# Performance work log

Hardware: AMD Instinct MI355X
Metric: run time of the kernel (lower is better)

Reference implementation:

```python
import jax, jax.numpy as jnp
import numpy as np

N_HEADS = 4
D_K = 64

def setup_inputs() -> dict:
    key = jax.random.key(0)
    k1, k2, k3 = jax.random.split(key, 3)
    B, C, H, W = 16, 256, 32, 32
    x = jax.random.normal(k1, (B, C, H, W), dtype=jnp.float32)
    # Linear(C, 3*n_heads*d_k) stored as [in, out] for x @ W
    w_proj = jax.random.normal(k2, (C, 3 * N_HEADS * D_K), dtype=jnp.float32) * (1.0 / np.sqrt(C))
    b_proj = jnp.zeros((3 * N_HEADS * D_K,), dtype=jnp.float32)
    w_out = jax.random.normal(k3, (N_HEADS * D_K, C), dtype=jnp.float32) * (1.0 / np.sqrt(N_HEADS * D_K))
    b_out = jnp.zeros((C,), dtype=jnp.float32)
    return {"x": x, "w_proj": w_proj, "b_proj": b_proj, "w_out": w_out, "b_out": b_out}

def reference(x, w_proj, b_proj, w_out, b_out):
    B, C, H, W = x.shape
    S = H * W
    scale = D_K ** -0.5
    xs = x.reshape(B, C, S).transpose(0, 2, 1)            # [B, S, C]
    qkv = (xs @ w_proj + b_proj).reshape(B, S, N_HEADS, 3 * D_K)
    q, k, v = jnp.split(qkv, 3, axis=3)                    # each [B, S, H, dk]
    attn = jnp.einsum('bihd,bjhd->bijh', q, k) * scale     # [B, S, S, heads]
    attn = jax.nn.softmax(attn, axis=2)
    o = jnp.einsum('bijh,bjhd->bihd', attn, v)             # [B, S, heads, dk]
    o = o.reshape(B, S, N_HEADS * D_K)
    res = o @ w_out + b_out + xs                           # [B, S, C]
    return res.transpose(0, 2, 1).reshape(B, C, H, W)
```

## Files before the change

kernel.cpp:

```cpp
#include <hip/hip_runtime.h>
#include <math.h>

#define B_  16
#define C_  256
#define S_  1024
#define NH  4
#define DK  64
#define P3  768
#define ND  256

typedef unsigned short u16;
typedef unsigned int   u32;
typedef float  f32x4  __attribute__((ext_vector_type(4)));
typedef short  bf16x8 __attribute__((ext_vector_type(8)));

#define MFMA16(a, b, c) __builtin_amdgcn_mfma_f32_16x16x32_bf16(a, b, c, 0, 0, 0)

#define QSCALE 0.1803368801111137f

#define WAITVM(N) asm volatile("s_waitcnt vmcnt(" #N ")" ::: "memory")
#define BARRIER() asm volatile("s_barrier" ::: "memory")

__device__ __forceinline__ u16 f2bf(float f) {
    union { float f; u32 u; } x; x.f = f;
    u32 r = x.u + 0x7fffu + ((x.u >> 16) & 1u);
    return (u16)(r >> 16);
}

__device__ __forceinline__ void stage16(const u16* g, u16* l) {
    __builtin_amdgcn_global_load_lds(
        (const __attribute__((address_space(1))) void*)g,
        (__attribute__((address_space(3))) void*)l, 16, 0, 0);
}

__global__ __launch_bounds__(256) void transpose_all(
    const float* __restrict__ x, u16* __restrict__ xt,
    const float* __restrict__ wp, u16* __restrict__ wpT,
    const float* __restrict__ wo, u16* __restrict__ woT)
{
    const int z = blockIdx.z;
    const float* src;
    u16* dst;
    int Cc;
    if (z < 16)       { src = x + (size_t)z * C_ * S_; dst = xt + (size_t)z * C_ * S_; Cc = S_; }
    else if (z == 16) { src = wp; dst = wpT; Cc = P3; }
    else              { src = wo; dst = woT; Cc = ND; }
    if ((int)blockIdx.x * 64 >= Cc) return;
    const int R = C_;

    __shared__ float T[64][65];
    const int tid = threadIdx.x;
    const int c0 = blockIdx.x * 64, r0 = blockIdx.y * 64;

    const int l64 = tid & 63, rr0 = tid >> 6;
    #pragma unroll
    for (int t = 0; t < 16; ++t) {
        int rr = rr0 + t * 4;
        T[rr][l64] = src[(size_t)(r0 + rr) * Cc + c0 + l64];
    }
    __syncthreads();
    const int rp = tid & 31;
    const int cb = tid >> 5;
    #pragma unroll
    for (int t = 0; t < 8; ++t) {
        int c = cb + t * 8;
        u32 lo = f2bf(T[2 * rp][c]);
        u32 hi = f2bf(T[2 * rp + 1][c]);
        *(u32*)&dst[(size_t)(c0 + c) * R + r0 + 2 * rp] = lo | (hi << 16);
    }
}

__global__ __launch_bounds__(256) void qkv_mfma(
    const u16* __restrict__ xt, const u16* __restrict__ wpT,
    const float* __restrict__ bp, u16* __restrict__ qo,
    u16* __restrict__ ko, u16* __restrict__ vo)
{
    __shared__ __align__(16) u16 SM[24576];

    const int tid = threadIdx.x;
    const int w = tid >> 6, lane = tid & 63;
    const int n_ = lane & 15, quad = lane >> 4;
    const int n0 = blockIdx.x * 64, s0 = blockIdx.y * 128, b = blockIdx.z;

    const u16* ar0 = xt + ((size_t)b * S_ + s0 + (2 * w + 0) * 16 + n_) * C_ + quad * 8;
    const u16* ar1 = xt + ((size_t)b * S_ + s0 + (2 * w + 1) * 16 + n_) * C_ + quad * 8;
    const u16* br  = wpT + (size_t)(n0 + w * 16 + n_) * C_ + quad * 8;

    f32x4 acc[2][4];
    #pragma unroll
    for (int am = 0; am < 2; ++am)
        #pragma unroll
        for (int nf = 0; nf < 4; ++nf)
            #pragma unroll
            for (int r = 0; r < 4; ++r) acc[am][nf][r] = 0.f;

    {
        u16* As_ = SM;
        u16* Bs_ = SM + 8192;
        stage16(ar0,      As_ + (4 * w + 0) * 512);
        stage16(ar0 + 32, As_ + (4 * w + 1) * 512);
        stage16(ar1,      As_ + (4 * w + 2) * 512);
        stage16(ar1 + 32, As_ + (4 * w + 3) * 512);
        stage16(br,       Bs_ + (2 * w + 0) * 512);
        stage16(br + 32,  Bs_ + (2 * w + 1) * 512);
    }

    #pragma unroll
    for (int p = 0; p < 4; ++p) {
        u16* As_ = SM + (p & 1) * 12288;
        u16* Bs_ = As_ + 8192;
        if (p < 3) {
            const int pk = (p + 1) * 64;
            u16* An = SM + ((p + 1) & 1) * 12288;
            u16* Bn = An + 8192;
            stage16(ar0 + pk,      An + (4 * w + 0) * 512);
            stage16(ar0 + pk + 32, An + (4 * w + 1) * 512);
            stage16(ar1 + pk,      An + (4 * w + 2) * 512);
            stage16(ar1 + pk + 32, An + (4 * w + 3) * 512);
            stage16(br  + pk,      Bn + (2 * w + 0) * 512);
            stage16(br  + pk + 32, Bn + (2 * w + 1) * 512);
            WAITVM(6);
        } else {
            WAITVM(0);
        }
        BARRIER();
        #pragma unroll
        for (int kc = 0; kc < 2; ++kc) {
            bf16x8 af0 = *(const bf16x8*)&As_[((2 * w + 0) * 2 + kc) * 512 + lane * 8];
            bf16x8 af1 = *(const bf16x8*)&As_[((2 * w + 1) * 2 + kc) * 512 + lane * 8];
            #pragma unroll
            for (int nf = 0; nf < 4; ++nf) {
                bf16x8 bf = *(const bf16x8*)&Bs_[(nf * 2 + kc) * 512 + lane * 8];
                acc[0][nf] = MFMA16(af0, bf, acc[0][nf]);
                acc[1][nf] = MFMA16(af1, bf, acc[1][nf]);
            }
        }
        if (p < 3) BARRIER();
    }

    const int hd = n0 / 192, rem = n0 % 192, which = rem / 64;
    const int bh = b * NH + hd;
    float bias[4];
    #pragma unroll
    for (int nf = 0; nf < 4; ++nf) bias[nf] = bp[n0 + nf * 16 + n_];
    const float sc = (which == 0) ? QSCALE : 1.f;

    __syncthreads();
    if (which < 2) {
        u16* Cs = SM;
        #pragma unroll
        for (int am = 0; am < 2; ++am) {
            int row0 = w * 32 + am * 16 + quad * 4;
            #pragma unroll
            for (int nf = 0; nf < 4; ++nf)
                #pragma unroll
                for (int r = 0; r < 4; ++r)
                    Cs[(row0 + r) * 72 + nf * 16 + n_] =
                        f2bf((acc[am][nf][r] + bias[nf]) * sc);
        }
        __syncthreads();
        u16* dst = (which == 0) ? qo : ko;
        #pragma unroll
        for (int t = 0; t < 4; ++t) {
            int ii = tid + t * 256;
            int row = ii >> 3, c8 = (ii & 7) * 8;
            *(bf16x8*)&dst[((size_t)bh * S_ + s0 + row) * DK + c8] =
                *(const bf16x8*)&Cs[row * 72 + c8];
        }
    } else {
        u16* Cs = SM;
        #pragma unroll
        for (int am = 0; am < 2; ++am) {
            int colb = w * 32 + am * 16 + quad * 4;
            #pragma unroll
            for (int nf = 0; nf < 4; ++nf)
                #pragma unroll
                for (int r = 0; r < 4; ++r)
                    Cs[(nf * 16 + n_) * 136 + colb + r] =
                        f2bf(acc[am][nf][r] + bias[nf]);
        }
        __syncthreads();
        #pragma unroll
        for (int t = 0; t < 4; ++t) {
            int ii = tid + t * 256;
            int row = ii >> 4, c8 = (ii & 15) * 8;
            *(bf16x8*)&vo[((size_t)bh * DK + row) * S_ + s0 + c8] =
                *(const bf16x8*)&Cs[row * 136 + c8];
        }
    }
}

__global__ __launch_bounds__(256) void attn_mfma(
    const u16* __restrict__ q, const u16* __restrict__ k,
    const u16* __restrict__ vt, u16* __restrict__ obf)
{
    __shared__ __align__(16) u16 SM[16384];

    const int tid = threadIdx.x;
    const int w = tid >> 6, lane = tid & 63;
    const int n_ = lane & 15, quad = lane >> 4;
    const int i0 = blockIdx.x * 128;
    const int hd = blockIdx.y, b = blockIdx.z;
    const int bh = b * NH + hd;

    bf16x8 qf[2][2];
    #pragma unroll
    for (int am = 0; am < 2; ++am) {
        const u16* qrow = q + ((size_t)bh * S_ + i0 + w * 32 + am * 16 + n_) * DK;
        qf[am][0] = *(const bf16x8*)&qrow[quad * 8];
        qf[am][1] = *(const bf16x8*)&qrow[32 + quad * 8];
    }

    const int kappa = 32 * (w & 1) + 8 * (n_ >> 2) + 4 * (w >> 1) + (n_ & 3);
    const u16* kbase = k  + ((size_t)bh * S_ + kappa) * DK + quad * 8;
    const u16* vbase = vt + ((size_t)bh * DK + w * 16 + n_) * S_ + quad * 8;

    float lsum[2] = {0.f, 0.f};
    f32x4 oacc[2][4];
    #pragma unroll
    for (int am = 0; am < 2; ++am)
        #pragma unroll
        for (int nd = 0; nd < 4; ++nd)
            #pragma unroll
            for (int r = 0; r < 4; ++r) oacc[am][nd][r] = 0.f;

    stage16(kbase,      SM + w * 1024);
    stage16(kbase + 32, SM + w * 1024 + 512);
    stage16(vbase,      SM + 4096 + w * 1024);
    stage16(vbase + 32, SM + 4096 + w * 1024 + 512);

    for (int t = 0; t < 16; ++t) {
        u16* Ks = SM + (t & 1) * 8192;
        u16* Vs = Ks + 4096;
        if (t < 15) {
            const size_t jn = (size_t)(t + 1) * 64;
            u16* Kn = SM + ((t + 1) & 1) * 8192;
            u16* Vn = Kn + 4096;
            stage16(kbase + jn * DK,      Kn + w * 1024);
            stage16(kbase + jn * DK + 32, Kn + w * 1024 + 512);
            stage16(vbase + jn,           Vn + w * 1024);
            stage16(vbase + jn + 32,      Vn + w * 1024 + 512);
            WAITVM(4);
        } else {
            WAITVM(0);
        }
        BARRIER();

        f32x4 sb[2][4];
        __builtin_amdgcn_s_setprio(1);
        #pragma unroll
        for (int nb = 0; nb < 4; ++nb) {
            bf16x8 kf0 = *(const bf16x8*)&Ks[nb * 1024 + lane * 8];
            bf16x8 kf1 = *(const bf16x8*)&Ks[nb * 1024 + 512 + lane * 8];
            #pragma unroll
            for (int am = 0; am < 2; ++am) {
                f32x4 a; a[0] = a[1] = a[2] = a[3] = 0.f;
                a = MFMA16(kf0, qf[am][0], a);
                a = MFMA16(kf1, qf[am][1], a);
                sb[am][nb] = a;
            }
        }
        __builtin_amdgcn_s_setprio(0);

        bf16x8 pa[2][2];
        #pragma unroll
        for (int am = 0; am < 2; ++am) {
            u32 tr[4][4];
            #pragma unroll
            for (int nb = 0; nb < 4; ++nb)
                #pragma unroll
                for (int r = 0; r < 4; ++r) {
                    float p = exp2f(sb[am][nb][r]);
                    u32 bits = __float_as_uint(p) & 0xffff0000u;
                    lsum[am] += __uint_as_float(bits);
                    tr[nb][r] = bits;
                }
            union { bf16x8 v; u32 u[4]; } p0, p1;
            p0.u[0] = (tr[0][0] >> 16) | tr[0][1];
            p0.u[1] = (tr[0][2] >> 16) | tr[0][3];
            p0.u[2] = (tr[2][0] >> 16) | tr[2][1];
            p0.u[3] = (tr[2][2] >> 16) | tr[2][3];
            p1.u[0] = (tr[1][0] >> 16) | tr[1][1];
            p1.u[1] = (tr[1][2] >> 16) | tr[1][3];
            p1.u[2] = (tr[3][0] >> 16) | tr[3][1];
            p1.u[3] = (tr[3][2] >> 16) | tr[3][3];
            pa[am][0] = p0.v;
            pa[am][1] = p1.v;
        }

        __builtin_amdgcn_s_setprio(1);
        #pragma unroll
        for (int nd = 0; nd < 4; ++nd) {
            bf16x8 vf0 = *(const bf16x8*)&Vs[nd * 1024 + lane * 8];
            bf16x8 vf1 = *(const bf16x8*)&Vs[nd * 1024 + 512 + lane * 8];
            #pragma unroll
            for (int am = 0; am < 2; ++am) {
                oacc[am][nd] = MFMA16(vf0, pa[am][0], oacc[am][nd]);
                oacc[am][nd] = MFMA16(vf1, pa[am][1], oacc[am][nd]);
            }
        }
        __builtin_amdgcn_s_setprio(0);

        if (t < 15) BARRIER();
    }

    float inv[2];
    #pragma unroll
    for (int am = 0; am < 2; ++am) {
        float s = lsum[am];
        s += __shfl_xor(s, 16);
        s += __shfl_xor(s, 32);
        inv[am] = 1.f / s;
    }

    __syncthreads();
    u16* eb = SM + w * 2304;
    #pragma unroll
    for (int am = 0; am < 2; ++am)
        #pragma unroll
        for (int nd = 0; nd < 4; ++nd) {
            uint2 uv;
            uv.x = (u32)f2bf(oacc[am][nd][0] * inv[am]) |
                   ((u32)f2bf(oacc[am][nd][1] * inv[am]) << 16);
            uv.y = (u32)f2bf(oacc[am][nd][2] * inv[am]) |
                   ((u32)f2bf(oacc[am][nd][3] * inv[am]) << 16);
            *(uint2*)&eb[(am * 16 + n_) * 72 + nd * 16 + quad * 4] = uv;
        }
    __syncthreads();
    #pragma unroll
    for (int t = 0; t < 4; ++t) {
        int ii = lane + t * 64;
        int row = ii >> 3, c8 = (ii & 7) * 8;
        *(bf16x8*)&obf[((size_t)b * S_ + i0 + w * 32 + row) * ND + hd * DK + c8] =
            *(const bf16x8*)&eb[row * 72 + c8];
    }
}

__global__ __launch_bounds__(256) void out_proj_mfma(
    const u16* __restrict__ obf, const u16* __restrict__ woT,
    const float* __restrict__ bo, const float* __restrict__ x,
    float* __restrict__ out)
{
    __shared__ __align__(16) u16 SM[24576];

    const int tid = threadIdx.x;
    const int w = tid >> 6, lane = tid & 63;
    const int n_ = lane & 15, quad = lane >> 4;
    const int c0 = blockIdx.x * 64, s0 = blockIdx.y * 128, b = blockIdx.z;

    const u16* ar  = woT + (size_t)(c0 + w * 16 + n_) * ND + quad * 8;
    const u16* br0 = obf + ((size_t)b * S_ + s0 + (2 * w + 0) * 16 + n_) * ND + quad * 8;
    const u16* br1 = obf + ((size_t)b * S_ + s0 + (2 * w + 1) * 16 + n_) * ND + quad * 8;

    f32x4 acc[2][4];
    #pragma unroll
    for (int nf = 0; nf < 2; ++nf)
        #pragma unroll
        for (int mb = 0; mb < 4; ++mb)
            #pragma unroll
            for (int r = 0; r < 4; ++r) acc[nf][mb][r] = 0.f;

    {
        u16* Bs_ = SM;
        u16* As_ = SM + 8192;
        stage16(br0,      Bs_ + (4 * w + 0) * 512);
        stage16(br0 + 32, Bs_ + (4 * w + 1) * 512);
        stage16(br1,      Bs_ + (4 * w + 2) * 512);
        stage16(br1 + 32, Bs_ + (4 * w + 3) * 512);
        stage16(ar,       As_ + (2 * w + 0) * 512);
        stage16(ar + 32,  As_ + (2 * w + 1) * 512);
    }

    #pragma unroll
    for (int p = 0; p < 4; ++p) {
        u16* Bs_ = SM + (p & 1) * 12288;
        u16* As_ = Bs_ + 8192;
        if (p < 3) {
            const int pk = (p + 1) * 64;
            u16* Bn = SM + ((p + 1) & 1) * 12288;
            u16* An = Bn + 8192;
            stage16(br0 + pk,      Bn + (4 * w + 0) * 512);
            stage16(br0 + pk + 32, Bn + (4 * w + 1) * 512);
            stage16(br1 + pk,      Bn + (4 * w + 2) * 512);
            stage16(br1 + pk + 32, Bn + (4 * w + 3) * 512);
            stage16(ar  + pk,      An + (2 * w + 0) * 512);
            stage16(ar  + pk + 32, An + (2 * w + 1) * 512);
            WAITVM(6);
        } else {
            WAITVM(0);
        }
        BARRIER();
        #pragma unroll
        for (int kc = 0; kc < 2; ++kc) {
            bf16x8 bf0 = *(const bf16x8*)&Bs_[((2 * w + 0) * 2 + kc) * 512 + lane * 8];
            bf16x8 bf1 = *(const bf16x8*)&Bs_[((2 * w + 1) * 2 + kc) * 512 + lane * 8];
            #pragma unroll
            for (int mb = 0; mb < 4; ++mb) {
                bf16x8 af = *(const bf16x8*)&As_[(mb * 2 + kc) * 512 + lane * 8];
                acc[0][mb] = MFMA16(af, bf0, acc[0][mb]);
                acc[1][mb] = MFMA16(af, bf1, acc[1][mb]);
            }
        }
        if (p < 3) BARRIER();
    }

    #pragma unroll
    for (int mb = 0; mb < 4; ++mb)
        #pragma unroll
        for (int r = 0; r < 4; ++r) {
            int c = c0 + mb * 16 + quad * 4 + r;
            float bias = bo[c];
            #pragma unroll
            for (int nf = 0; nf < 2; ++nf) {
                size_t idx = ((size_t)b * C_ + c) * S_ + s0 + w * 32 + nf * 16 + n_;
                out[idx] = acc[nf][mb][r] + bias + x[idx];
            }
        }
}

extern "C" void kernel_launch(void* const* d_in, const int* in_sizes, int n_in,
                              void* d_out, int out_size, void* d_ws, size_t ws_size,
                              hipStream_t stream) {
    const float* x  = (const float*)d_in[0];
    const float* wp = (const float*)d_in[1];
    const float* bp = (const float*)d_in[2];
    const float* wo = (const float*)d_in[3];
    const float* bo = (const float*)d_in[4];
    float* out = (float*)d_out;

    const size_t QKV_E = (size_t)B_ * NH * S_ * DK;
    u16* q   = (u16*)d_ws;
    u16* kk  = q   + QKV_E;
    u16* vtp = kk  + QKV_E;
    u16* obf = vtp + QKV_E;
    u16* xt  = obf + (size_t)B_ * S_ * ND;
    u16* wpT = xt  + (size_t)B_ * S_ * C_;
    u16* woT = wpT + (size_t)P3 * C_;

    transpose_all<<<dim3(16, 4, 18),             256, 0, stream>>>(x, xt, wp, wpT, wo, woT);
    qkv_mfma     <<<dim3(P3 / 64, S_ / 128, B_), 256, 0, stream>>>(xt, wpT, bp, q, kk, vtp);
    attn_mfma    <<<dim3(S_ / 128, NH, B_),      256, 0, stream>>>(q, kk, vtp, obf);
    out_proj_mfma<<<dim3(C_ / 64, S_ / 128, B_), 256, 0, stream>>>(obf, woT, bo, x, out);
}
```

Baseline: 139.8 us.

## Halve attention query tile to 64 rows, remap blocks per XCD, use packed bf16 convert

Each attention block now handles 64 query rows instead of 128, so each wave owns one 16-row tile and 1024 blocks are launched on a 1D grid. The block index is permuted so consecutive blocks sharing the same (batch, head) K/V land on the same XCD, aiming at better L2 reuse and more parallelism. The manual bf16 truncation and rounding are replaced with the v_cvt_pk_bf16_f32 instruction, and the softmax sum now uses unrounded probabilities. The trade-off is that K/V tiles are loaded twice as often per query row and each wave has less MFMA work per LDS load.

```diff
diff --git a/kernel.cpp b/kernel.cpp
--- a/kernel.cpp
+++ b/kernel.cpp
@@ -25,6 +25,12 @@
     union { float f; u32 u; } x; x.f = f;
     u32 r = x.u + 0x7fffu + ((x.u >> 16) & 1u);
     return (u16)(r >> 16);
+}
+
+__device__ __forceinline__ u32 cvtpk(float lo, float hi) {
+    u32 r;
+    asm("v_cvt_pk_bf16_f32 %0, %1, %2" : "=v"(r) : "v"(lo), "v"(hi));
+    return r;
 }
 
 __device__ __forceinline__ void stage16(const u16* g, u16* l) {
@@ -199,30 +205,31 @@
     const int tid = threadIdx.x;
     const int w = tid >> 6, lane = tid & 63;
     const int n_ = lane & 15, quad = lane >> 4;
-    const int i0 = blockIdx.x * 128;
-    const int hd = blockIdx.y, b = blockIdx.z;
-    const int bh = b * NH + hd;
-
-    bf16x8 qf[2][2];
-    #pragma unroll
-    for (int am = 0; am < 2; ++am) {
-        const u16* qrow = q + ((size_t)bh * S_ + i0 + w * 32 + am * 16 + n_) * DK;
-        qf[am][0] = *(const bf16x8*)&qrow[quad * 8];
-        qf[am][1] = *(const bf16x8*)&qrow[32 + quad * 8];
+
+    const int id  = blockIdx.x;
+    const int nid = (id & 7) * 128 + (id >> 3);
+    const int i0  = (nid & 15) * 64;
+    const int hd  = (nid >> 4) & 3;
+    const int b   = nid >> 6;
+    const int bh  = b * NH + hd;
+
+    bf16x8 qf[2];
+    {
+        const u16* qrow = q + ((size_t)bh * S_ + i0 + w * 16 + n_) * DK;
+        qf[0] = *(const bf16x8*)&qrow[quad * 8];
+        qf[1] = *(const bf16x8*)&qrow[32 + quad * 8];
     }
 
     const int kappa = 32 * (w & 1) + 8 * (n_ >> 2) + 4 * (w >> 1) + (n_ & 3);
     const u16* kbase = k  + ((size_t)bh * S_ + kappa) * DK + quad * 8;
     const u16* vbase = vt + ((size_t)bh * DK + w * 16 + n_) * S_ + quad * 8;
 
-    float lsum[2] = {0.f, 0.f};
-    f32x4 oacc[2][4];
-    #pragma unroll
-    for (int am = 0; am < 2; ++am)
-        #pragma unroll
-        for (int nd = 0; nd < 4; ++nd)
-            #pragma unroll
-            for (int r = 0; r < 4; ++r) oacc[am][nd][r] = 0.f;
+    float lsum = 0.f;
+    f32x4 oacc[4];
+    #pragma unroll
+    for (int nd = 0; nd < 4; ++nd)
+        #pragma unroll
+        for (int r = 0; r < 4; ++r) oacc[nd][r] = 0.f;
 
     stage16(kbase,      SM + w * 1024);
     stage16(kbase + 32, SM + w * 1024 + 512);
@@ -246,46 +253,41 @@
         }
         BARRIER();
 
-        f32x4 sb[2][4];
+        f32x4 sb[4];
         __builtin_amdgcn_s_setprio(1);
         #pragma unroll
         for (int nb = 0; nb < 4; ++nb) {
             bf16x8 kf0 = *(const bf16x8*)&Ks[nb * 1024 + lane * 8];
             bf16x8 kf1 = *(const bf16x8*)&Ks[nb * 1024 + 512 + lane * 8];
-            #pragma unroll
-            for (int am = 0; am < 2; ++am) {
-                f32x4 a; a[0] = a[1] = a[2] = a[3] = 0.f;
-                a = MFMA16(kf0, qf[am][0], a);
-                a = MFMA16(kf1, qf[am][1], a);
-                sb[am][nb] = a;
+            f32x4 a; a[0] = a[1] = a[2] = a[3] = 0.f;
+            a = MFMA16(kf0, qf[0], a);
+            a = MFMA16(kf1, qf[1], a);
+            sb[nb] = a;
+        }
+        __builtin_amdgcn_s_setprio(0);
+
+        float pr[4][4];
+        #pragma unroll
+        for (int nb = 0; nb < 4; ++nb)
+            #pragma unroll
+            for (int r = 0; r < 4; ++r) {
+                float p = exp2f(sb[nb][r]);
+                lsum += p;
+                pr[nb][r] = p;
             }
-        }
-        __builtin_amdgcn_s_setprio(0);
-
-        bf16x8 pa[2][2];
-        #pragma unroll
-        for (int am = 0; am < 2; ++am) {
-            u32 tr[4][4];
-            #pragma unroll
-            for (int nb = 0; nb < 4; ++nb)
-                #pragma unroll
-                for (int r = 0; r < 4; ++r) {
-                    float p = exp2f(sb[am][nb][r]);
-                    u32 bits = __float_as_uint(p) & 0xffff0000u;
-                    lsum[am] += __uint_as_float(bits);
-                    tr[nb][r] = bits;
-                }
+        bf16x8 pa[2];
+        {
             union { bf16x8 v; u32 u[4]; } p0, p1;
-            p0.u[0] = (tr[0][0] >> 16) | tr[0][1];
-            p0.u[1] = (tr[0][2] >> 16) | tr[0][3];
-            p0.u[2] = (tr[2][0] >> 16) | tr[2][1];
-            p0.u[3] = (tr[2][2] >> 16) | tr[2][3];
-            p1.u[0] = (tr[1][0] >> 16) | tr[1][1];
-            p1.u[1] = (tr[1][2] >> 16) | tr[1][3];
-            p1.u[2] = (tr[3][0] >> 16) | tr[3][1];
-            p1.u[3] = (tr[3][2] >> 16) | tr[3][3];
-            pa[am][0] = p0.v;
-            pa[am][1] = p1.v;
+            p0.u[0] = cvtpk(pr[0][0], pr[0][1]);
+            p0.u[1] = cvtpk(pr[0][2], pr[0][3]);
+            p0.u[2] = cvtpk(pr[2][0], pr[2][1]);
+            p0.u[3] = cvtpk(pr[2][2], pr[2][3]);
+            p1.u[0] = cvtpk(pr[1][0], pr[1][1]);
+            p1.u[1] = cvtpk(pr[1][2], pr[1][3]);
+            p1.u[2] = cvtpk(pr[3][0], pr[3][1]);
+            p1.u[3] = cvtpk(pr[3][2], pr[3][3]);
+            pa[0] = p0.v;
+            pa[1] = p1.v;
         }
 
         __builtin_amdgcn_s_setprio(1);
@@ -293,45 +295,34 @@
         for (int nd = 0; nd < 4; ++nd) {
             bf16x8 vf0 = *(const bf16x8*)&Vs[nd * 1024 + lane * 8];
             bf16x8 vf1 = *(const bf16x8*)&Vs[nd * 1024 + 512 + lane * 8];
-            #pragma unroll
-            for (int am = 0; am < 2; ++am) {
-                oacc[am][nd] = MFMA16(vf0, pa[am][0], oacc[am][nd]);
-                oacc[am][nd] = MFMA16(vf1, pa[am][1], oacc[am][nd]);
-            }
+            oacc[nd] = MFMA16(vf0, pa[0], oacc[nd]);
+            oacc[nd] = MFMA16(vf1, pa[1], oacc[nd]);
         }
         __builtin_amdgcn_s_setprio(0);
 
         if (t < 15) BARRIER();
     }
 
-    float inv[2];
-    #pragma unroll
-    for (int am = 0; am < 2; ++am) {
-        float s = lsum[am];
-        s += __shfl_xor(s, 16);
-        s += __shfl_xor(s, 32);
-        inv[am] = 1.f / s;
-    }
+    float s = lsum;
+    s += __shfl_xor(s, 16);
+    s += __shfl_xor(s, 32);
+    const float inv = 1.f / s;
 
     __syncthreads();
-    u16* eb = SM + w * 2304;
-    #pragma unroll
-    for (int am = 0; am < 2; ++am)
-        #pragma unroll
-        for (int nd = 0; nd < 4; ++nd) {
-            uint2 uv;
-            uv.x = (u32)f2bf(oacc[am][nd][0] * inv[am]) |
-                   ((u32)f2bf(oacc[am][nd][1] * inv[am]) << 16);
-            uv.y = (u32)f2bf(oacc[am][nd][2] * inv[am]) |
-                   ((u32)f2bf(oacc[am][nd][3] * inv[am]) << 16);
-            *(uint2*)&eb[(am * 16 + n_) * 72 + nd * 16 + quad * 4] = uv;
-        }
+    u16* eb = SM + w * 1152;
+    #pragma unroll
+    for (int nd = 0; nd < 4; ++nd) {
+        uint2 uv;
+        uv.x = cvtpk(oacc[nd][0] * inv, oacc[nd][1] * inv);
+        uv.y = cvtpk(oacc[nd][2] * inv, oacc[nd][3] * inv);
+        *(uint2*)&eb[n_ * 72 + nd * 16 + quad * 4] = uv;
+    }
     __syncthreads();
     #pragma unroll
-    for (int t = 0; t < 4; ++t) {
+    for (int t = 0; t < 2; ++t) {
         int ii = lane + t * 64;
         int row = ii >> 3, c8 = (ii & 7) * 8;
-        *(bf16x8*)&obf[((size_t)b * S_ + i0 + w * 32 + row) * ND + hd * DK + c8] =
+        *(bf16x8*)&obf[((size_t)b * S_ + i0 + w * 16 + row) * ND + hd * DK + c8] =
             *(const bf16x8*)&eb[row * 72 + c8];
     }
 }
@@ -439,6 +430,6 @@
 
     transpose_all<<<dim3(16, 4, 18),             256, 0, stream>>>(x, xt, wp, wpT, wo, woT);
     qkv_mfma     <<<dim3(P3 / 64, S_ / 128, B_), 256, 0, stream>>>(xt, wpT, bp, q, kk, vtp);
-    attn_mfma    <<<dim3(S_ / 128, NH, B_),      256, 0, stream>>>(q, kk, vtp, obf);
+    attn_mfma    <<<dim3(1024, 1, 1),            256, 0, stream>>>(q, kk, vtp, obf);
     out_proj_mfma<<<dim3(C_ / 64, S_ / 128, B_), 256, 0, stream>>>(obf, woT, bo, x, out);
 }
```

After: 144.0 us. +3.0%, slower.

## Deepen attention K/V prefetch to four buffers, drop barrier, remap blocks, use packed bf16 convert

Applied to the files above, without the earlier changes.

The attention kernel now keeps four LDS buffers for K/V tiles and prefetches two tiles ahead. This lets it remove the trailing per-iteration barrier, since a buffer is only refilled two iterations after it was read. The grid is flattened to 1D with an XCD-aware remap so the eight query blocks of one batch-head land on the same XCD, which should improve L2 reuse of K/V. The manual truncation to bf16 is replaced by the hardware v_cvt_pk_bf16_f32 instruction, which rounds rather than truncates, so lsum now accumulates unrounded probabilities. In exchange, LDS use doubles to 64KB per block, which may reduce occupancy.

```diff
diff --git a/kernel.cpp b/kernel.cpp
--- a/kernel.cpp
+++ b/kernel.cpp
@@ -25,6 +25,12 @@
     union { float f; u32 u; } x; x.f = f;
     u32 r = x.u + 0x7fffu + ((x.u >> 16) & 1u);
     return (u16)(r >> 16);
+}
+
+__device__ __forceinline__ u32 cvtpk(float lo, float hi) {
+    u32 r;
+    asm("v_cvt_pk_bf16_f32 %0, %1, %2" : "=v"(r) : "v"(lo), "v"(hi));
+    return r;
 }
 
 __device__ __forceinline__ void stage16(const u16* g, u16* l) {
@@ -194,14 +200,18 @@
     const u16* __restrict__ q, const u16* __restrict__ k,
     const u16* __restrict__ vt, u16* __restrict__ obf)
 {
-    __shared__ __align__(16) u16 SM[16384];
+    __shared__ __align__(16) u16 SM[32768];
 
     const int tid = threadIdx.x;
     const int w = tid >> 6, lane = tid & 63;
     const int n_ = lane & 15, quad = lane >> 4;
-    const int i0 = blockIdx.x * 128;
-    const int hd = blockIdx.y, b = blockIdx.z;
-    const int bh = b * NH + hd;
+
+    const int id  = blockIdx.x;
+    const int nid = (id & 7) * 64 + (id >> 3);
+    const int i0  = (nid & 7) * 128;
+    const int bh  = nid >> 3;
+    const int hd  = bh & 3;
+    const int b   = bh >> 2;
 
     bf16x8 qf[2][2];
     #pragma unroll
@@ -224,22 +234,28 @@
             #pragma unroll
             for (int r = 0; r < 4; ++r) oacc[am][nd][r] = 0.f;
 
-    stage16(kbase,      SM + w * 1024);
-    stage16(kbase + 32, SM + w * 1024 + 512);
-    stage16(vbase,      SM + 4096 + w * 1024);
-    stage16(vbase + 32, SM + 4096 + w * 1024 + 512);
+    stage16(kbase,                SM + w * 1024);
+    stage16(kbase + 32,           SM + w * 1024 + 512);
+    stage16(vbase,                SM + 4096 + w * 1024);
+    stage16(vbase + 32,           SM + 4096 + w * 1024 + 512);
+    stage16(kbase + 64 * DK,      SM + 8192 + w * 1024);
+    stage16(kbase + 64 * DK + 32, SM + 8192 + w * 1024 + 512);
+    stage16(vbase + 64,           SM + 8192 + 4096 + w * 1024);
+    stage16(vbase + 64 + 32,      SM + 8192 + 4096 + w * 1024 + 512);
 
     for (int t = 0; t < 16; ++t) {
-        u16* Ks = SM + (t & 1) * 8192;
+        u16* Ks = SM + (t & 3) * 8192;
         u16* Vs = Ks + 4096;
-        if (t < 15) {
-            const size_t jn = (size_t)(t + 1) * 64;
-            u16* Kn = SM + ((t + 1) & 1) * 8192;
+        if (t < 14) {
+            const size_t jn = (size_t)(t + 2) * 64;
+            u16* Kn = SM + ((t + 2) & 3) * 8192;
             u16* Vn = Kn + 4096;
             stage16(kbase + jn * DK,      Kn + w * 1024);
             stage16(kbase + jn * DK + 32, Kn + w * 1024 + 512);
             stage16(vbase + jn,           Vn + w * 1024);
             stage16(vbase + jn + 32,      Vn + w * 1024 + 512);
+            WAITVM(8);
+        } else if (t == 14) {
             WAITVM(4);
         } else {
             WAITVM(0);
@@ -265,25 +281,24 @@
         bf16x8 pa[2][2];
         #pragma unroll
         for (int am = 0; am < 2; ++am) {
-            u32 tr[4][4];
+            float pr[4][4];
             #pragma unroll
             for (int nb = 0; nb < 4; ++nb)
                 #pragma unroll
                 for (int r = 0; r < 4; ++r) {
                     float p = exp2f(sb[am][nb][r]);
-                    u32 bits = __float_as_uint(p) & 0xffff0000u;
-                    lsum[am] += __uint_as_float(bits);
-                    tr[nb][r] = bits;
+                    lsum[am] += p;
+                    pr[nb][r] = p;
                 }
             union { bf16x8 v; u32 u[4]; } p0, p1;
-            p0.u[0] = (tr[0][0] >> 16) | tr[0][1];
-            p0.u[1] = (tr[0][2] >> 16) | tr[0][3];
-            p0.u[2] = (tr[2][0] >> 16) | tr[2][1];
-            p0.u[3] = (tr[2][2] >> 16) | tr[2][3];
-            p1.u[0] = (tr[1][0] >> 16) | tr[1][1];
-            p1.u[1] = (tr[1][2] >> 16) | tr[1][3];
-            p1.u[2] = (tr[3][0] >> 16) | tr[3][1];
-            p1.u[3] = (tr[3][2] >> 16) | tr[3][3];
+            p0.u[0] = cvtpk(pr[0][0], pr[0][1]);
+            p0.u[1] = cvtpk(pr[0][2], pr[0][3]);
+            p0.u[2] = cvtpk(pr[2][0], pr[2][1]);
+            p0.u[3] = cvtpk(pr[2][2], pr[2][3]);
+            p1.u[0] = cvtpk(pr[1][0], pr[1][1]);
+            p1.u[1] = cvtpk(pr[1][2], pr[1][3]);
+            p1.u[2] = cvtpk(pr[3][0], pr[3][1]);
+            p1.u[3] = cvtpk(pr[3][2], pr[3][3]);
             pa[am][0] = p0.v;
             pa[am][1] = p1.v;
         }
@@ -300,8 +315,6 @@
             }
         }
         __builtin_amdgcn_s_setprio(0);
-
-        if (t < 15) BARRIER();
     }
 
     float inv[2];
@@ -320,10 +333,8 @@
         #pragma unroll
         for (int nd = 0; nd < 4; ++nd) {
             uint2 uv;
-            uv.x = (u32)f2bf(oacc[am][nd][0] * inv[am]) |
-                   ((u32)f2bf(oacc[am][nd][1] * inv[am]) << 16);
-            uv.y = (u32)f2bf(oacc[am][nd][2] * inv[am]) |
-                   ((u32)f2bf(oacc[am][nd][3] * inv[am]) << 16);
+            uv.x = cvtpk(oacc[am][nd][0] * inv[am], oacc[am][nd][1] * inv[am]);
+            uv.y = cvtpk(oacc[am][nd][2] * inv[am], oacc[am][nd][3] * inv[am]);
             *(uint2*)&eb[(am * 16 + n_) * 72 + nd * 16 + quad * 4] = uv;
         }
     __syncthreads();
@@ -439,6 +450,6 @@
 
     transpose_all<<<dim3(16, 4, 18),             256, 0, stream>>>(x, xt, wp, wpT, wo, woT);
     qkv_mfma     <<<dim3(P3 / 64, S_ / 128, B_), 256, 0, stream>>>(xt, wpT, bp, q, kk, vtp);
-    attn_mfma    <<<dim3(S_ / 128, NH, B_),      256, 0, stream>>>(q, kk, vtp, obf);
+    attn_mfma    <<<dim3(512, 1, 1),             256, 0, stream>>>(q, kk, vtp, obf);
     out_proj_mfma<<<dim3(C_ / 64, S_ / 128, B_), 256, 0, stream>>>(obf, woT, bo, x, out);
 }
```

New measurement: 139.9 us. No clear change (+0.1%).
